# Kernel tuning notes

Hardware: AMD Instinct MI355X
Metric: run time of the kernel (lower is better)

The kernel has to match this reference:

```python
import jax, jax.numpy as jnp
import numpy as np

N_NODES = 100000
N_EDGES = 1600000
D = 128  # in_feats = n_hidden = out_feats


def _linear_params(key, d_in, d_out):
    kw, kb = jax.random.split(key)
    scale = 1.0 / np.sqrt(d_in)
    W = jax.random.uniform(kw, (d_in, d_out), jnp.float32, -scale, scale)
    b = jax.random.uniform(kb, (d_out,), jnp.float32, -scale, scale)
    return W, b


def setup_inputs() -> dict:
    key = jax.random.key(0)
    keys = jax.random.split(key, 8)
    x = jax.random.normal(keys[0], (N_NODES, D), jnp.float32)
    edge_index = jax.random.randint(keys[1], (2, N_EDGES), 0, N_NODES, jnp.int64)
    inp = {"x": x, "edge_index": edge_index}
    for l in range(3):
        W1, b1 = _linear_params(keys[2 + 2 * l], D, D)
        W2, b2 = _linear_params(keys[3 + 2 * l], D, D)
        inp[f"W1_{l}"] = W1
        inp[f"b1_{l}"] = b1
        inp[f"W2_{l}"] = W2
        inp[f"b2_{l}"] = b2
    return inp


def _gin_conv(x, src, dst, W1, b1, W2, b2):
    # GINConv: MLP((1+eps)*x + sum_{j->i} x_j), eps=0
    agg = jax.ops.segment_sum(x[src], dst, num_segments=N_NODES)
    h = agg + x
    h = jnp.maximum(h @ W1 + b1, 0.0)
    return h @ W2 + b2


def reference(x, edge_index, W1_0, b1_0, W2_0, b2_0,
              W1_1, b1_1, W2_1, b2_1, W1_2, b1_2, W2_2, b2_2):
    src, dst = edge_index[0], edge_index[1]
    # layer 0 (loop body): conv -> relu
    x = jnp.maximum(_gin_conv(x, src, dst, W1_0, b1_0, W2_0, b2_0), 0.0)
    # layer 1 (num_layers-2): conv -> relu -> dropout (eval: identity)
    x = jnp.maximum(_gin_conv(x, src, dst, W1_1, b1_1, W2_1, b2_1), 0.0)
    # layer 2 (last): conv -> relu
    x = jnp.maximum(_gin_conv(x, src, dst, W1_2, b1_2, W2_2, b2_2), 0.0)
    return x
```

## Files before the change

### kernel.cpp

```cpp
#include <hip/hip_runtime.h>

#define N_NODES 100000
#define N_EDGES 1600000
#define D 128
#define NBUCK 98
#define CAP 20480
#define PCAP 24576

typedef __attribute__((ext_vector_type(8))) short bf16x8;
typedef __attribute__((ext_vector_type(4))) float f32x4;
typedef unsigned long long u64;

__device__ __forceinline__ float b2f_lo(unsigned int u) {
    return __builtin_bit_cast(float, u << 16);
}
__device__ __forceinline__ float b2f_hi(unsigned int u) {
    return __builtin_bit_cast(float, u & 0xFFFF0000u);
}
__device__ __forceinline__ unsigned short f2b(float f) {
    unsigned int u = __builtin_bit_cast(unsigned int, f);
    u += 0x7FFFu + ((u >> 16) & 1u);
    return (unsigned short)(u >> 16);
}


__global__ __launch_bounds__(256) void prep_kernel(
    const float* __restrict__ x, unsigned short* __restrict__ xb,
    const float* __restrict__ W0, const float* __restrict__ W1_, const float* __restrict__ W2_,
    const float* __restrict__ W3, const float* __restrict__ W4, const float* __restrict__ W5,
    unsigned short* __restrict__ T0, unsigned short* __restrict__ T1_,
    unsigned short* __restrict__ T2_, unsigned short* __restrict__ T3,
    unsigned short* __restrict__ T4, unsigned short* __restrict__ T5,
    uint4* __restrict__ dob4, uint4* __restrict__ xs0) {
    int blk = blockIdx.x;
    if (blk < 384) {
        const float* W;
        unsigned short* T;
        switch (blk >> 6) {
            case 0: W = W0; T = T0; break;
            case 1: W = W1_; T = T1_; break;
            case 2: W = W2_; T = T2_; break;
            case 3: W = W3; T = T3; break;
            case 4: W = W4; T = T4; break;
            default: W = W5; T = T5; break;
        }
        int i = (blk & 63) * 256 + threadIdx.x;
        int k = i >> 7, n = i & 127;
        T[n * 128 + k] = f2b(W[i]);
    } else if (blk < 12884) {
        int i = (blk - 384) * 256 + threadIdx.x;
        if (i < 3200000) {
            float4 v = ((const float4*)x)[i];
            ushort4 o;
            o.x = f2b(v.x); o.y = f2b(v.y); o.z = f2b(v.z); o.w = f2b(v.w);
            ((ushort4*)xb)[i] = o;
        }
    } else {
        int i = (blk - 12884) * 256 + threadIdx.x;
        uint4 z = {0u, 0u, 0u, 0u};
        if (i < 256) dob4[i] = z;
        if (i < 16) xs0[i] = z;
    }
}


__global__ __launch_bounds__(256) void bin_kernel(const int* __restrict__ src,
                                                  const int* __restrict__ dst,
                                                  int* __restrict__ bcur,
                                                  u64* __restrict__ ebuf) {
    __shared__ int h[NBUCK];
    __shared__ int base[NBUCK];
    int tid = threadIdx.x;
    if (tid < NBUCK) h[tid] = 0;
    __syncthreads();
    int e0 = blockIdx.x * 2048;
    int myd[8], mys[8];
#pragma unroll
    for (int i = 0; i < 8; i++) {
        int e = e0 + tid + i * 256;
        int dv = (e < N_EDGES) ? dst[e] : -1;
        myd[i] = dv;
        mys[i] = (e < N_EDGES) ? src[e] : 0;
        if (dv >= 0) atomicAdd(&h[dv >> 10], 1);
    }
    __syncthreads();
    if (tid < NBUCK) {
        int c = h[tid];
        base[tid] = (c > 0) ? (tid * CAP + atomicAdd(&bcur[tid], c)) : 0;
        h[tid] = 0;
    }
    __syncthreads();
#pragma unroll
    for (int i = 0; i < 8; i++) {
        int dv = myd[i];
        if (dv >= 0) {
            int b = dv >> 10;
            int p = base[b] + atomicAdd(&h[b], 1);
            if (p < (b + 1) * CAP)
                ebuf[p] = ((u64)(unsigned int)dv << 32) | (unsigned int)mys[i];
        }
    }
}

__global__ __launch_bounds__(1024) void bucket_all_kernel(const u64* __restrict__ ebuf,
                                                          const int* __restrict__ bcur,
                                                          int* __restrict__ off,
                                                          int* __restrict__ offe,
                                                          int* __restrict__ csr) {
    __shared__ int hist[1024];
    __shared__ int sc[1024];
    __shared__ int cnt[1024];
    int b = blockIdx.x, tid = threadIdx.x;
    int nE = bcur[b]; if (nE > CAP) nE = CAP;
    int base = b * PCAP;
    const u64* slab = ebuf + (size_t)b * CAP;
    hist[tid] = 0;
    cnt[tid] = 0;
    __syncthreads();
    for (int i = tid; i < nE; i += 1024)
        atomicAdd(&hist[(int)(slab[i] >> 32) & 1023], 1);
    __syncthreads();
    int node = b * 1024 + tid;
    int d = hist[tid];
    int dp = (node < N_NODES) ? ((d + 3) & ~3) : 0;
    sc[tid] = dp;
    __syncthreads();
#pragma unroll
    for (int s = 1; s < 1024; s <<= 1) {
        int t = (tid >= s) ? sc[tid - s] : 0;
        __syncthreads();
        sc[tid] += t;
        __syncthreads();
    }
    int excl = sc[tid] - dp;
    sc[tid] = excl;
    if (node < N_NODES) {
        off[node] = base + excl;
        offe[node] = base + excl + dp;
    }
    __syncthreads();
    for (int i = tid; i < nE; i += 1024) {
        u64 e = slab[i];
        int dd = (int)(e >> 32) & 1023;
        int pos = sc[dd] + atomicAdd(&cnt[dd], 1);
        csr[base + pos] = (int)(e & 0xFFFFFFFFu);
    }
    for (int j = d; j < dp; j++) csr[base + excl + j] = N_NODES;
}


__global__ __launch_bounds__(256) void agg_bf16(const unsigned int* __restrict__ xb,
                                                const int* __restrict__ off,
                                                const int* __restrict__ offe,
                                                const int* __restrict__ csr,
                                                unsigned int* __restrict__ t) {
    int node = blockIdx.x * 4 + (threadIdx.x >> 6);
    int lane = threadIdx.x & 63;
    unsigned int v = xb[(size_t)node * 64 + lane];
    float ax = b2f_lo(v), ay = b2f_hi(v);
    int k = off[node], e = offe[node];
    for (; k + 8 <= e; k += 8) {
        int n0 = csr[k + 0], n1 = csr[k + 1], n2 = csr[k + 2], n3 = csr[k + 3];
        int n4 = csr[k + 4], n5 = csr[k + 5], n6 = csr[k + 6], n7 = csr[k + 7];
        unsigned int g0 = xb[(size_t)n0 * 64 + lane];
        unsigned int g1 = xb[(size_t)n1 * 64 + lane];
        unsigned int g2 = xb[(size_t)n2 * 64 + lane];
        unsigned int g3 = xb[(size_t)n3 * 64 + lane];
        unsigned int g4 = xb[(size_t)n4 * 64 + lane];
        unsigned int g5 = xb[(size_t)n5 * 64 + lane];
        unsigned int g6 = xb[(size_t)n6 * 64 + lane];
        unsigned int g7 = xb[(size_t)n7 * 64 + lane];
        ax += b2f_lo(g0) + b2f_lo(g1) + b2f_lo(g2) + b2f_lo(g3)
            + b2f_lo(g4) + b2f_lo(g5) + b2f_lo(g6) + b2f_lo(g7);
        ay += b2f_hi(g0) + b2f_hi(g1) + b2f_hi(g2) + b2f_hi(g3)
            + b2f_hi(g4) + b2f_hi(g5) + b2f_hi(g6) + b2f_hi(g7);
    }
    if (k < e) {
        int n0 = csr[k + 0], n1 = csr[k + 1], n2 = csr[k + 2], n3 = csr[k + 3];
        unsigned int g0 = xb[(size_t)n0 * 64 + lane];
        unsigned int g1 = xb[(size_t)n1 * 64 + lane];
        unsigned int g2 = xb[(size_t)n2 * 64 + lane];
        unsigned int g3 = xb[(size_t)n3 * 64 + lane];
        ax += b2f_lo(g0) + b2f_lo(g1) + b2f_lo(g2) + b2f_lo(g3);
        ay += b2f_hi(g0) + b2f_hi(g1) + b2f_hi(g2) + b2f_hi(g3);
    }
    t[(size_t)node * 64 + lane] = (unsigned int)f2b(ax) | ((unsigned int)f2b(ay) << 16);
}


template <bool OUT_F32>
__global__ __launch_bounds__(256) void mlp_mfma(const unsigned short* __restrict__ A,
                                                const unsigned short* __restrict__ W1t,
                                                const float* __restrict__ bias1,
                                                const unsigned short* __restrict__ W2t,
                                                const float* __restrict__ bias2,
                                                void* __restrict__ out) {
    __shared__ char smem[4 * 8704];
    int tid = threadIdx.x;
    int wave = tid >> 6, lane = tid & 63;
    int quad = lane >> 4, mr = lane & 15;
    int m_base = blockIdx.x * 128 + wave * 32;
    int m0 = m_base + mr;       if (m0 >= N_NODES) m0 = N_NODES - 1;
    int m1 = m_base + 16 + mr;  if (m1 >= N_NODES) m1 = N_NODES - 1;

    unsigned short* ust = (unsigned short*)(smem + wave * 8704);

    bf16x8 a0[4], a1[4];
#pragma unroll
    for (int kc = 0; kc < 4; kc++) {
        a0[kc] = *(const bf16x8*)(A + (size_t)m0 * D + kc * 32 + quad * 8);
        a1[kc] = *(const bf16x8*)(A + (size_t)m1 * D + kc * 32 + quad * 8);
    }

    f32x4 acc0[8], acc1[8];
#pragma unroll
    for (int nt = 0; nt < 8; nt++) { acc0[nt] = (f32x4)0.0f; acc1[nt] = (f32x4)0.0f; }
#pragma unroll
    for (int nt = 0; nt < 8; nt++) {
        const unsigned short* wp = W1t + (size_t)(nt * 16 + mr) * D + quad * 8;
#pragma unroll
        for (int kc = 0; kc < 4; kc++) {
            bf16x8 b = *(const bf16x8*)(wp + kc * 32);
            acc0[nt] = __builtin_amdgcn_mfma_f32_16x16x32_bf16(a0[kc], b, acc0[nt], 0, 0, 0);
            acc1[nt] = __builtin_amdgcn_mfma_f32_16x16x32_bf16(a1[kc], b, acc1[nt], 0, 0, 0);
        }
    }
#pragma unroll
    for (int nt = 0; nt < 8; nt++) {
        float bv = bias1[nt * 16 + mr];
#pragma unroll
        for (int r = 0; r < 4; r++) {
            ust[(quad * 4 + r) * 136 + nt * 16 + mr] = f2b(fmaxf(acc0[nt][r] + bv, 0.0f));
            ust[2176 + (quad * 4 + r) * 136 + nt * 16 + mr] = f2b(fmaxf(acc1[nt][r] + bv, 0.0f));
        }
    }

#pragma unroll
    for (int kc = 0; kc < 4; kc++) {
        a0[kc] = *(const bf16x8*)&ust[mr * 136 + kc * 32 + quad * 8];
        a1[kc] = *(const bf16x8*)&ust[2176 + mr * 136 + kc * 32 + quad * 8];
    }
#pragma unroll
    for (int nt = 0; nt < 8; nt++) { acc0[nt] = (f32x4)0.0f; acc1[nt] = (f32x4)0.0f; }
#pragma unroll
    for (int nt = 0; nt < 8; nt++) {
        const unsigned short* wp = W2t + (size_t)(nt * 16 + mr) * D + quad * 8;
#pragma unroll
        for (int kc = 0; kc < 4; kc++) {
            bf16x8 b = *(const bf16x8*)(wp + kc * 32);
            acc0[nt] = __builtin_amdgcn_mfma_f32_16x16x32_bf16(a0[kc], b, acc0[nt], 0, 0, 0);
            acc1[nt] = __builtin_amdgcn_mfma_f32_16x16x32_bf16(a1[kc], b, acc1[nt], 0, 0, 0);
        }
    }

    if (OUT_F32) {
        float* st = (float*)ust;
        const int S = 132;
        float* op = (float*)out;
#pragma unroll
        for (int s = 0; s < 2; s++) {
#pragma unroll
            for (int nt = 0; nt < 8; nt++) {
                float bv = bias2[nt * 16 + mr];
#pragma unroll
                for (int r = 0; r < 4; r++) {
                    float v = s ? acc1[nt][r] : acc0[nt][r];
                    st[(quad * 4 + r) * S + nt * 16 + mr] = fmaxf(v + bv, 0.0f);
                }
            }
#pragma unroll
            for (int it = 0; it < 8; it++) {
                int linear = lane + it * 64;
                int row = linear >> 5, col = (linear & 31) << 2;
                int gm = m_base + s * 16 + row;
                if (gm < N_NODES) {
                    float4 val = *(float4*)&st[row * S + col];
                    *(float4*)(op + (size_t)gm * D + col) = val;
                }
            }
        }
    } else {
        const int S = 136;
        unsigned short* op = (unsigned short*)out;
#pragma unroll
        for (int s = 0; s < 2; s++) {
            unsigned short* st = ust + s * 2176;
#pragma unroll
            for (int nt = 0; nt < 8; nt++) {
                float bv = bias2[nt * 16 + mr];
#pragma unroll
                for (int r = 0; r < 4; r++) {
                    float v = s ? acc1[nt][r] : acc0[nt][r];
                    st[(quad * 4 + r) * S + nt * 16 + mr] = f2b(fmaxf(v + bv, 0.0f));
                }
            }
#pragma unroll
            for (int it = 0; it < 4; it++) {
                int linear = lane + it * 64;
                int row = linear >> 4, col = (linear & 15) << 3;
                int gm = m_base + s * 16 + row;
                if (gm < N_NODES) {
                    uint4 val = *(uint4*)&st[row * S + col];
                    *(uint4*)(op + (size_t)gm * D + col) = val;
                }
            }
        }
    }
}


extern "C" void kernel_launch(void* const* d_in, const int* in_sizes, int n_in,
                              void* d_out, int out_size, void* d_ws, size_t ws_size,
                              hipStream_t stream) {
    const float* x = (const float*)d_in[0];
    const int* ei = (const int*)d_in[1];
    const int* srcv = ei;
    const int* dstv = ei + N_EDGES;
    const float* W1[3] = {(const float*)d_in[2], (const float*)d_in[6], (const float*)d_in[10]};
    const float* b1[3] = {(const float*)d_in[3], (const float*)d_in[7], (const float*)d_in[11]};
    const float* W2[3] = {(const float*)d_in[4], (const float*)d_in[8], (const float*)d_in[12]};
    const float* b2[3] = {(const float*)d_in[5], (const float*)d_in[9], (const float*)d_in[13]};

    char* ws = (char*)d_ws;
    int* off  = (int*)ws;
    int* offe = (int*)(ws + 400000);
    unsigned short* Wt[6];
    for (int i = 0; i < 6; i++) Wt[i] = (unsigned short*)(ws + 800000 + i * 32768);
    unsigned short* xb = (unsigned short*)(ws + 1048576);
    unsigned short* P  = (unsigned short*)(ws + 26648832);

    char* dob = (char*)d_out;
    int* bcur = (int*)(dob);
    u64* ebuf = (u64*)(dob + 1048576);
    int* csr  = (int*)(dob + 17104896);

    prep_kernel<<<12885, 256, 0, stream>>>(
        x, xb,
        W1[0], W2[0], W1[1], W2[1], W1[2], W2[2],
        Wt[0], Wt[1], Wt[2], Wt[3], Wt[4], Wt[5],
        (uint4*)dob, (uint4*)(xb + (size_t)N_NODES * D));

    bin_kernel<<<782, 256, 0, stream>>>(srcv, dstv, bcur, ebuf);
    bucket_all_kernel<<<NBUCK, 1024, 0, stream>>>(ebuf, bcur, off, offe, csr);

    const int agg_grid = 25000;
    const int mlp_grid = (N_NODES + 127) / 128;

    agg_bf16<<<agg_grid, 256, 0, stream>>>((const unsigned int*)xb, off, offe, csr, (unsigned int*)P);
    mlp_mfma<false><<<mlp_grid, 256, 0, stream>>>(P, Wt[0], b1[0], Wt[1], b2[0], xb);
    agg_bf16<<<agg_grid, 256, 0, stream>>>((const unsigned int*)xb, off, offe, csr, (unsigned int*)P);
    mlp_mfma<false><<<mlp_grid, 256, 0, stream>>>(P, Wt[2], b1[1], Wt[3], b2[1], xb);
    agg_bf16<<<agg_grid, 256, 0, stream>>>((const unsigned int*)xb, off, offe, csr, (unsigned int*)P);
    mlp_mfma<true><<<mlp_grid, 256, 0, stream>>>(P, Wt[4], b1[2], Wt[5], b2[2], d_out);
}
```

Measured before the change: 488.8 us.

## Pre-swizzle MLP weights into MFMA fragment order, unroll gather to 16, shrink MLP blocks

Weights are written in the prep kernel directly in MFMA B-fragment order, so each lane loads one contiguous 16-byte chunk per tile instead of strided rows. The aggregation loop batches 16 neighbour indices and gathers per iteration, with 8 and 4 tails, to keep more loads in flight. The MLP kernel now uses 128-thread blocks covering 64 rows over 1563 blocks, halving shared memory per block for better occupancy and tail balance. The wider gather raises register pressure, and the changes mix layout, unrolling and launch shape.

```diff
diff --git a/kernel.cpp b/kernel.cpp
--- a/kernel.cpp
+++ b/kernel.cpp
@@ -46,7 +46,9 @@
         }
         int i = (blk & 63) * 256 + threadIdx.x;
         int k = i >> 7, n = i & 127;
-        T[n * 128 + k] = f2b(W[i]);
+        int nt = n >> 4, mr = n & 15;
+        int kc = k >> 5, rem = k & 31, quad = rem >> 3, j = rem & 7;
+        T[(nt * 4 + kc) * 512 + quad * 128 + mr * 8 + j] = f2b(W[i]);
     } else if (blk < 12884) {
         int i = (blk - 384) * 256 + threadIdx.x;
         if (i < 3200000) {
@@ -159,47 +161,53 @@
     unsigned int v = xb[(size_t)node * 64 + lane];
     float ax = b2f_lo(v), ay = b2f_hi(v);
     int k = off[node], e = offe[node];
-    for (; k + 8 <= e; k += 8) {
-        int n0 = csr[k + 0], n1 = csr[k + 1], n2 = csr[k + 2], n3 = csr[k + 3];
-        int n4 = csr[k + 4], n5 = csr[k + 5], n6 = csr[k + 6], n7 = csr[k + 7];
-        unsigned int g0 = xb[(size_t)n0 * 64 + lane];
-        unsigned int g1 = xb[(size_t)n1 * 64 + lane];
-        unsigned int g2 = xb[(size_t)n2 * 64 + lane];
-        unsigned int g3 = xb[(size_t)n3 * 64 + lane];
-        unsigned int g4 = xb[(size_t)n4 * 64 + lane];
-        unsigned int g5 = xb[(size_t)n5 * 64 + lane];
-        unsigned int g6 = xb[(size_t)n6 * 64 + lane];
-        unsigned int g7 = xb[(size_t)n7 * 64 + lane];
-        ax += b2f_lo(g0) + b2f_lo(g1) + b2f_lo(g2) + b2f_lo(g3)
-            + b2f_lo(g4) + b2f_lo(g5) + b2f_lo(g6) + b2f_lo(g7);
-        ay += b2f_hi(g0) + b2f_hi(g1) + b2f_hi(g2) + b2f_hi(g3)
-            + b2f_hi(g4) + b2f_hi(g5) + b2f_hi(g6) + b2f_hi(g7);
+    for (; k + 16 <= e; k += 16) {
+        int idx[16];
+        unsigned int g[16];
+#pragma unroll
+        for (int i = 0; i < 16; i++) idx[i] = csr[k + i];
+#pragma unroll
+        for (int i = 0; i < 16; i++) g[i] = xb[(size_t)idx[i] * 64 + lane];
+#pragma unroll
+        for (int i = 0; i < 16; i++) { ax += b2f_lo(g[i]); ay += b2f_hi(g[i]); }
+    }
+    if (k + 8 <= e) {
+        int idx[8];
+        unsigned int g[8];
+#pragma unroll
+        for (int i = 0; i < 8; i++) idx[i] = csr[k + i];
+#pragma unroll
+        for (int i = 0; i < 8; i++) g[i] = xb[(size_t)idx[i] * 64 + lane];
+#pragma unroll
+        for (int i = 0; i < 8; i++) { ax += b2f_lo(g[i]); ay += b2f_hi(g[i]); }
+        k += 8;
     }
     if (k < e) {
-        int n0 = csr[k + 0], n1 = csr[k + 1], n2 = csr[k + 2], n3 = csr[k + 3];
-        unsigned int g0 = xb[(size_t)n0 * 64 + lane];
-        unsigned int g1 = xb[(size_t)n1 * 64 + lane];
-        unsigned int g2 = xb[(size_t)n2 * 64 + lane];
-        unsigned int g3 = xb[(size_t)n3 * 64 + lane];
-        ax += b2f_lo(g0) + b2f_lo(g1) + b2f_lo(g2) + b2f_lo(g3);
-        ay += b2f_hi(g0) + b2f_hi(g1) + b2f_hi(g2) + b2f_hi(g3);
+        int idx[4];
+        unsigned int g[4];
+#pragma unroll
+        for (int i = 0; i < 4; i++) idx[i] = csr[k + i];
+#pragma unroll
+        for (int i = 0; i < 4; i++) g[i] = xb[(size_t)idx[i] * 64 + lane];
+#pragma unroll
+        for (int i = 0; i < 4; i++) { ax += b2f_lo(g[i]); ay += b2f_hi(g[i]); }
     }
     t[(size_t)node * 64 + lane] = (unsigned int)f2b(ax) | ((unsigned int)f2b(ay) << 16);
 }
 
 
 template <bool OUT_F32>
-__global__ __launch_bounds__(256) void mlp_mfma(const unsigned short* __restrict__ A,
-                                                const unsigned short* __restrict__ W1t,
+__global__ __launch_bounds__(128) void mlp_mfma(const unsigned short* __restrict__ A,
+                                                const unsigned short* __restrict__ W1f,
                                                 const float* __restrict__ bias1,
-                                                const unsigned short* __restrict__ W2t,
+                                                const unsigned short* __restrict__ W2f,
                                                 const float* __restrict__ bias2,
                                                 void* __restrict__ out) {
-    __shared__ char smem[4 * 8704];
+    __shared__ char smem[2 * 8704];
     int tid = threadIdx.x;
     int wave = tid >> 6, lane = tid & 63;
     int quad = lane >> 4, mr = lane & 15;
-    int m_base = blockIdx.x * 128 + wave * 32;
+    int m_base = blockIdx.x * 64 + wave * 32;
     int m0 = m_base + mr;       if (m0 >= N_NODES) m0 = N_NODES - 1;
     int m1 = m_base + 16 + mr;  if (m1 >= N_NODES) m1 = N_NODES - 1;
 
@@ -217,10 +225,9 @@
     for (int nt = 0; nt < 8; nt++) { acc0[nt] = (f32x4)0.0f; acc1[nt] = (f32x4)0.0f; }
 #pragma unroll
     for (int nt = 0; nt < 8; nt++) {
-        const unsigned short* wp = W1t + (size_t)(nt * 16 + mr) * D + quad * 8;
 #pragma unroll
         for (int kc = 0; kc < 4; kc++) {
-            bf16x8 b = *(const bf16x8*)(wp + kc * 32);
+            bf16x8 b = *(const bf16x8*)(W1f + (nt * 4 + kc) * 512 + lane * 8);
             acc0[nt] = __builtin_amdgcn_mfma_f32_16x16x32_bf16(a0[kc], b, acc0[nt], 0, 0, 0);
             acc1[nt] = __builtin_amdgcn_mfma_f32_16x16x32_bf16(a1[kc], b, acc1[nt], 0, 0, 0);
         }
@@ -244,10 +251,9 @@
     for (int nt = 0; nt < 8; nt++) { acc0[nt] = (f32x4)0.0f; acc1[nt] = (f32x4)0.0f; }
 #pragma unroll
     for (int nt = 0; nt < 8; nt++) {
-        const unsigned short* wp = W2t + (size_t)(nt * 16 + mr) * D + quad * 8;
 #pragma unroll
         for (int kc = 0; kc < 4; kc++) {
-            bf16x8 b = *(const bf16x8*)(wp + kc * 32);
+            bf16x8 b = *(const bf16x8*)(W2f + (nt * 4 + kc) * 512 + lane * 8);
             acc0[nt] = __builtin_amdgcn_mfma_f32_16x16x32_bf16(a0[kc], b, acc0[nt], 0, 0, 0);
             acc1[nt] = __builtin_amdgcn_mfma_f32_16x16x32_bf16(a1[kc], b, acc1[nt], 0, 0, 0);
         }
@@ -344,12 +350,12 @@
     bucket_all_kernel<<<NBUCK, 1024, 0, stream>>>(ebuf, bcur, off, offe, csr);
 
     const int agg_grid = 25000;
-    const int mlp_grid = (N_NODES + 127) / 128;
+    const int mlp_grid = 1563;
 
     agg_bf16<<<agg_grid, 256, 0, stream>>>((const unsigned int*)xb, off, offe, csr, (unsigned int*)P);
-    mlp_mfma<false><<<mlp_grid, 256, 0, stream>>>(P, Wt[0], b1[0], Wt[1], b2[0], xb);
+    mlp_mfma<false><<<mlp_grid, 128, 0, stream>>>(P, Wt[0], b1[0], Wt[1], b2[0], xb);
     agg_bf16<<<agg_grid, 256, 0, stream>>>((const unsigned int*)xb, off, offe, csr, (unsigned int*)P);
-    mlp_mfma<false><<<mlp_grid, 256, 0, stream>>>(P, Wt[2], b1[1], Wt[3], b2[1], xb);
+    mlp_mfma<false><<<mlp_grid, 128, 0, stream>>>(P, Wt[2], b1[1], Wt[3], b2[1], xb);
     agg_bf16<<<agg_grid, 256, 0, stream>>>((const unsigned int*)xb, off, offe, csr, (unsigned int*)P);
-    mlp_mfma<true><<<mlp_grid, 256, 0, stream>>>(P, Wt[4], b1[2], Wt[5], b2[2], d_out);
-}
+    mlp_mfma<true><<<mlp_grid, 128, 0, stream>>>(P, Wt[4], b1[2], Wt[5], b2[2], d_out);
+}
```

Result: faster. 414.5 us (-15.2%).
